# Optimization experiments

Hardware: AMD Instinct MI355X
Metric: run time of the kernel (lower is better)

The kernel has to match this reference:

```python
import jax, jax.numpy as jnp
import numpy as np

B, S, D_IN, D_OUT = 2, 4096, 512, 512


def setup_inputs() -> dict:
    key = jax.random.key(0)
    k1, k2, k3, k4 = jax.random.split(key, 4)
    x = jax.random.normal(k1, (B, S, D_IN), dtype=jnp.float32)
    # weights stored as [d_in, d_out] so projection is x @ W
    W_query = jax.random.normal(k2, (D_IN, D_OUT), dtype=jnp.float32) * (D_IN ** -0.5)
    W_key = jax.random.normal(k3, (D_IN, D_OUT), dtype=jnp.float32) * (D_IN ** -0.5)
    W_value = jax.random.normal(k4, (D_IN, D_OUT), dtype=jnp.float32) * (D_IN ** -0.5)
    return {"x": x, "W_query": W_query, "W_key": W_key, "W_value": W_value}


def reference(x, W_query, W_key, W_value):
    # Faithful to source: masked_fill is called non-in-place and its result
    # discarded, so NO causal mask is actually applied. Dropout prob = 0.0.
    d_out = W_query.shape[-1]
    q = jnp.einsum('bsi,io->bso', x, W_query)  # [B,S,D_OUT]
    k = jnp.einsum('bsi,io->bso', x, W_key)
    v = jnp.einsum('bsi,io->bso', x, W_value)
    scores = jnp.einsum('bqd,bkd->bqk', q, k) / jnp.sqrt(jnp.float32(d_out))
    weights = jax.nn.softmax(scores, axis=-1)  # [B,S,S]
    context = jnp.einsum('bqk,bkd->bqd', weights, v)  # [B,S,D_OUT]
    return context
```

## Files before the change

kernel.cpp:

```cpp
#include <hip/hip_runtime.h>
#include <cstdint>
#include <cstddef>

typedef unsigned short u16;
typedef __attribute__((ext_vector_type(8))) short bf16x8;
typedef __attribute__((ext_vector_type(4))) float f32x4;

struct alignas(8) u16x4_t { u16 x, y, z, w; };

__device__ __forceinline__ u16 f2bf(float f) {
  uint32_t u = __builtin_bit_cast(uint32_t, f);
  u += 0x7FFFu + ((u >> 16) & 1u);
  return (u16)(u >> 16);
}
__device__ __forceinline__ float bf2f(u16 h) {
  uint32_t u = ((uint32_t)h) << 16;
  return __builtin_bit_cast(float, u);
}

__device__ __forceinline__ void g2l16(const u16* g, u16* l) {
  __builtin_amdgcn_global_load_lds(
      (const __attribute__((address_space(1))) void*)g,
      (__attribute__((address_space(3))) void*)l, 16, 0, 0);
}

#define S_WAITCNT_VM(N) \
  __builtin_amdgcn_s_waitcnt((((N) & 0xF)) | (0x7 << 4) | (0xF << 8) | ((((N) >> 4) & 3) << 14))
#define S_WAITCNT_LGKM0 __builtin_amdgcn_s_waitcnt(0xC07F)

template <int DEPTH, int BM, int BN>
__device__ __forceinline__ void gemm_bt_pipe(
    const u16* __restrict__ A, const u16* __restrict__ Bt,
    int lda, int ldb, int kIters, int m0, int n0,
    u16* sh, f32x4 (&acc)[BM / 32][BN / 32]) {
  constexpr int MI = BM / 32;
  constexpr int NI = BN / 32;
  constexpr int T = (BM + BN) / 64;
  constexpr int SLOT = (BM + BN) * 32;
  const int tid = threadIdx.x;
  const int lane = tid & 63, wave = tid >> 6;
  const int wm = wave >> 1, wn = wave & 1, lr = lane & 15, quad = lane >> 4;

  const u16* gp[T];
#pragma unroll
  for (int t = 0; t < T; ++t) {
    const int c = t * 256 + wave * 64 + lane;
    if (c < BM * 4) {
      const int r = c >> 2;
      const int s = (c & 3) ^ ((r >> 1) & 3);
      gp[t] = A + (size_t)(m0 + r) * lda + s * 8;
    } else {
      const int cb = c - BM * 4;
      const int r = cb >> 2;
      const int s = (cb & 3) ^ ((r >> 1) & 3);
      gp[t] = Bt + (size_t)(n0 + r) * ldb + s * 8;
    }
  }
  const int wo = wave * 512;

  auto issue = [&](int slot, int kb) {
    u16* s = sh + slot * SLOT;
#pragma unroll
    for (int t = 0; t < T; ++t)
      g2l16(gp[t] + kb, s + t * 2048 + wo);
  };

#pragma unroll
  for (int p = 0; p < DEPTH; ++p)
    issue(p, (p < kIters ? p : kIters - 1) * 32);

  const int xq = (quad ^ ((lr >> 1) & 3)) * 8;
  const int arow = wm * (BM / 2) + lr;
  const int brow = wn * (BN / 2) + lr;

  bf16x8 af[MI], b0[NI], b1[NI];
  S_WAITCNT_VM(T * (DEPTH - 1));
  __builtin_amdgcn_s_barrier();
#pragma unroll
  for (int ni = 0; ni < NI; ++ni)
    b0[ni] = *(const bf16x8*)(sh + BM * 32 + ((brow + ni * 16) * 32 + xq));
#pragma unroll
  for (int mi = 0; mi < MI; ++mi)
    af[mi] = *(const bf16x8*)(sh + ((arow + mi * 16) * 32 + xq));

  auto step = [&](int kt, bf16x8 (&bc)[NI], bf16x8 (&bn)[NI]) {
    S_WAITCNT_VM(T * (DEPTH - 2));
    __builtin_amdgcn_s_barrier();
    const int nx = (kt + 1 < kIters) ? kt + 1 : kIters - 1;
    u16* s1 = sh + (nx % DEPTH) * SLOT;
#pragma unroll
    for (int ni = 0; ni < NI; ++ni)
      bn[ni] = *(const bf16x8*)(s1 + BM * 32 + ((brow + ni * 16) * 32 + xq));
    __builtin_amdgcn_s_setprio(1);
#pragma unroll
    for (int mi = 0; mi < MI; ++mi) {
#pragma unroll
      for (int ni = 0; ni < NI; ++ni)
        acc[mi][ni] = __builtin_amdgcn_mfma_f32_16x16x32_bf16(af[mi], bc[ni], acc[mi][ni], 0, 0, 0);
      af[mi] = *(const bf16x8*)(s1 + ((arow + mi * 16) * 32 + xq));
    }
    __builtin_amdgcn_s_setprio(0);
    __builtin_amdgcn_s_barrier();
    const int kn = kt + DEPTH;
    issue(kn % DEPTH, (kn < kIters ? kn : kIters - 1) * 32);
  };

  for (int kt = 0; kt + 2 <= kIters; kt += 2) {
    step(kt, b0, b1);
    step(kt + 1, b1, b0);
  }
}

template <int BM, int BN>
__device__ __forceinline__ void gemm_bt_8w_4ph(
    const u16* __restrict__ A, const u16* __restrict__ Bt,
    int lda, int ldb, int kIters, int m0, int n0,
    u16* sh, f32x4 (&acc)[BM / 32][BN / 64]) {
  constexpr int T = (BM + BN) / 128;
  constexpr int SLOT = (BM + BN) * 32;
  const int tid = threadIdx.x;
  const int lane = tid & 63, wave = tid >> 6;
  const int wm = wave >> 2, wn = wave & 3, lr = lane & 15, quad = lane >> 4;

  const u16* gp[T];
#pragma unroll
  for (int t = 0; t < T; ++t) {
    const int c = t * 512 + wave * 64 + lane;
    if (c < BM * 4) {
      const int r = c >> 2;
      const int s = (c & 3) ^ ((r >> 1) & 3);
      gp[t] = A + (size_t)(m0 + r) * lda + s * 8;
    } else {
      const int cb = c - BM * 4;
      const int r = cb >> 2;
      const int s = (cb & 3) ^ ((r >> 1) & 3);
      gp[t] = Bt + (size_t)(n0 + r) * ldb + s * 8;
    }
  }
  const int wo = wave * 512;

#pragma unroll
  for (int p = 0; p < 2; ++p)
#pragma unroll
    for (int t = 0; t < T; ++t)
      g2l16(gp[t] + p * 32, sh + p * SLOT + t * 4096 + wo);
  S_WAITCNT_VM(4);
  __builtin_amdgcn_s_barrier();

  const int xq = (quad ^ ((lr >> 1) & 3)) * 8;
  const int abase = (wm * (BM / 2) + lr) * 32 + xq;
  const int bbase = BM * 32 + (wn * (BN / 4) + lr) * 32 + xq;

  int si = 0, s2 = 2;
  for (int kt = 0; kt < kIters; ++kt) {
    u16* slot = sh + si * SLOT;
    const int kn = kt + 2;
    const int kb = (kn < kIters ? kn : kIters - 1) * 32;
    u16* st = sh + s2 * SLOT + wo;

    bf16x8 a0[4], b0[4];
#pragma unroll
    for (int i = 0; i < 4; ++i)
      a0[i] = *(const bf16x8*)(slot + abase + i * 512);
#pragma unroll
    for (int j = 0; j < 4; ++j)
      b0[j] = *(const bf16x8*)(slot + bbase + j * 512);
    g2l16(gp[0] + kb, st);
    g2l16(gp[1] + kb, st + 4096);
    __builtin_amdgcn_s_barrier();
    S_WAITCNT_LGKM0;
    __builtin_amdgcn_s_setprio(1);
#pragma unroll
    for (int i = 0; i < 4; ++i)
#pragma unroll
      for (int j = 0; j < 4; ++j)
        acc[i][j] = __builtin_amdgcn_mfma_f32_16x16x32_bf16(a0[i], b0[j], acc[i][j], 0, 0, 0);
    __builtin_amdgcn_s_setprio(0);
    __builtin_amdgcn_s_barrier();
#pragma unroll
    for (int i = 0; i < 4; ++i)
      a0[i] = *(const bf16x8*)(slot + abase + (4 + i) * 512);
    g2l16(gp[2] + kb, st + 8192);
    g2l16(gp[3] + kb, st + 12288);
    __builtin_amdgcn_s_barrier();
    S_WAITCNT_LGKM0;
    __builtin_amdgcn_s_setprio(1);
#pragma unroll
    for (int i = 0; i < 4; ++i)
#pragma unroll
      for (int j = 0; j < 4; ++j)
        acc[4 + i][j] = __builtin_amdgcn_mfma_f32_16x16x32_bf16(a0[i], b0[j], acc[4 + i][j], 0, 0, 0);
    __builtin_amdgcn_s_setprio(0);
    S_WAITCNT_VM(4);
    __builtin_amdgcn_s_barrier();
    si = si == 2 ? 0 : si + 1;
    s2 = s2 == 2 ? 0 : s2 + 1;
  }
}

#define ZERO_ACC4(acc)                        \
  _Pragma("unroll") for (int mi = 0; mi < 4; ++mi) \
  _Pragma("unroll") for (int ni = 0; ni < 4; ++ni) \
      acc[mi][ni] = f32x4{0.f, 0.f, 0.f, 0.f};

template <int MI>
__device__ __forceinline__ void epilogue_ct16(
    const f32x4 (&acc)[MI][4], u16* __restrict__ base, int m0w, int n0w,
    int ld, int lane, bool do_exp, float scale, float* rs) {
  const int lr = lane & 15, quad = lane >> 4;
  const int j = quad >> 1, par = quad & 1;
#pragma unroll
  for (int mp = 0; mp < MI / 2; ++mp) {
#pragma unroll
    for (int ni = 0; ni < 4; ++ni) {
      uint32_t p0[2], p1[2];
#pragma unroll
      for (int h = 0; h < 2; ++h) {
        const f32x4 v = acc[mp * 2 + h][ni];
        float e0, e1, e2, e3;
        if (do_exp) {
          e0 = __expf(v[0] * scale); e1 = __expf(v[1] * scale);
          e2 = __expf(v[2] * scale); e3 = __expf(v[3] * scale);
        } else {
          e0 = v[0]; e1 = v[1]; e2 = v[2]; e3 = v[3];
        }
        const u16 h0 = f2bf(e0), h1 = f2bf(e1), h2 = f2bf(e2), h3 = f2bf(e3);
        p0[h] = (uint32_t)h0 | ((uint32_t)h1 << 16);
        p1[h] = (uint32_t)h2 | ((uint32_t)h3 << 16);
        if (rs) rs[ni] += bf2f(h0) + bf2f(h1) + bf2f(h2) + bf2f(h3);
      }
      const uint32_t s0 = par ? p0[0] : p0[1];
      const uint32_t s1 = par ? p1[0] : p1[1];
      const uint32_t r0 = (uint32_t)__shfl_xor((int)s0, 16);
      const uint32_t r1 = (uint32_t)__shfl_xor((int)s1, 16);
      uint4 st;
      if (!par) { st.x = p0[0]; st.y = p1[0]; st.z = r0;    st.w = r1;    }
      else      { st.x = r0;    st.y = r1;    st.z = p0[1]; st.w = p1[1]; }
      const int m = m0w + 16 * (mp * 2 + par) + 8 * j;
      const int n = n0w + ni * 16 + lr;
      *(uint4*)(base + (size_t)n * ld + m) = st;
    }
  }
}

__global__ __launch_bounds__(256) void prep_kernel(
    const float* __restrict__ x, u16* __restrict__ Xb,
    const float* __restrict__ W0, const float* __restrict__ W1,
    const float* __restrict__ W2, u16* __restrict__ Wt,
    float* __restrict__ L) {
  __shared__ float tile[32][33];
  const int id = blockIdx.x;
  if (id < 4096) {
    const int i = (id * 256 + threadIdx.x) * 4;
    const float4 v = *(const float4*)(x + i);
    u16x4_t h;
    h.x = f2bf(v.x); h.y = f2bf(v.y); h.z = f2bf(v.z); h.w = f2bf(v.w);
    *(u16x4_t*)(Xb + i) = h;
    return;
  }
  if (id >= 4864) {
    L[(id - 4864) * 256 + threadIdx.x] = 0.f;
    return;
  }
  const int t = id - 4096;
  const int wz = t >> 8, rem = t & 255;
  const float* W = wz == 0 ? W0 : (wz == 1 ? W1 : W2);
  u16* out = Wt + (size_t)wz * 512 * 512;
  const int bx = (rem & 15) * 32;
  const int by = (rem >> 4) * 32;
  const int tx = threadIdx.x & 31, ty = threadIdx.x >> 5;
#pragma unroll
  for (int i = 0; i < 32; i += 8)
    tile[ty + i][tx] = W[(size_t)(by + ty + i) * 512 + bx + tx];
  __syncthreads();
#pragma unroll
  for (int i = 0; i < 32; i += 8)
    out[(size_t)(bx + ty + i) * 512 + by + tx] = f2bf(tile[tx][ty + i]);
}

__global__ __launch_bounds__(256) void qkv_kernel(
    const u16* __restrict__ Xb, const u16* __restrict__ Wt,
    u16* __restrict__ Qb, u16* __restrict__ Kb, u16* __restrict__ Vt) {
  __shared__ u16 sh[3 * 8192];
  const int z = blockIdx.z;
  int m0, n0;
  const u16 *A, *Bt;
  if (z < 2) {
    m0 = blockIdx.y * 128;
    n0 = blockIdx.x * 128;
    A = Wt + (size_t)z * 512 * 512;
    Bt = Xb;
  } else {
    m0 = blockIdx.x * 128;
    n0 = blockIdx.y * 128;
    A = Xb;
    Bt = Wt + (size_t)2 * 512 * 512;
  }
  f32x4 acc[4][4];
  ZERO_ACC4(acc);
  gemm_bt_pipe<3, 128, 128>(A, Bt, 512, 512, 16, m0, n0, sh, acc);

  const int lane = threadIdx.x & 63, wave = threadIdx.x >> 6;
  const int wm = wave >> 1, wn = wave & 1;
  if (z < 2) {
    epilogue_ct16<4>(acc, z == 0 ? Qb : Kb, m0 + wm * 64, n0 + wn * 64, 512,
                     lane, false, 1.f, nullptr);
  } else {
    const int bb = m0 >> 12;
    epilogue_ct16<4>(acc, Vt + (size_t)bb * 512 * 4096,
                     (m0 & 4095) + wm * 64, n0 + wn * 64, 4096,
                     lane, false, 1.f, nullptr);
  }
}

__global__ __launch_bounds__(512, 2) void scores_kernel(
    const u16* __restrict__ Qb, const u16* __restrict__ Kb,
    u16* __restrict__ P, float* __restrict__ L) {
  extern __shared__ u16 sh[];
  const int id = blockIdx.x;
  const int b = id >> 8;
  const int r = id & 255;
  const int j = r >> 3;
  const int qx = (r & 7) * 2 + (j >> 4);
  const int ky = j & 15;
  const int m0 = ky * 256;
  const int n0 = qx * 256;
  f32x4 acc[8][4];
#pragma unroll
  for (int mi = 0; mi < 8; ++mi)
#pragma unroll
    for (int ni = 0; ni < 4; ++ni)
      acc[mi][ni] = f32x4{0.f, 0.f, 0.f, 0.f};
  gemm_bt_8w_4ph<256, 256>(Kb + (size_t)b * 4096 * 512,
                           Qb + (size_t)b * 4096 * 512,
                           512, 512, 16, m0, n0, sh, acc);

  const int lane = threadIdx.x & 63, wave = threadIdx.x >> 6;
  const int wm = wave >> 2, wn = wave & 3, lr = lane & 15, quad = lane >> 4;
  const float scale = 0.04419417382415922f;
  u16* Pb = P + (size_t)b * 4096 * 4096;

  float rs[4] = {0.f, 0.f, 0.f, 0.f};
  epilogue_ct16<8>(acc, Pb, m0 + wm * 128, n0 + wn * 64, 4096, lane, true,
                   scale, rs);

#pragma unroll
  for (int ni = 0; ni < 4; ++ni) {
    float v = rs[ni];
    v += __shfl_xor(v, 16);
    v += __shfl_xor(v, 32);
    if (quad == 0)
      atomicAdd(&L[b * 4096 + n0 + wn * 64 + ni * 16 + lr], v);
  }
}

__global__ __launch_bounds__(256) void pv_kernel(
    const u16* __restrict__ P, const u16* __restrict__ Vt,
    float* __restrict__ part0, float* __restrict__ out) {
  __shared__ u16 sh[3 * 8192];
  const int b = blockIdx.z;
  const int id = blockIdx.x;
  const int ntile = (id >> 3) & 3;
  const int rest = (id & 7) | ((id >> 5) << 3);
  const int mtile = rest & 31;
  const int ks = rest >> 5;
  const int m0 = mtile * 128;
  const int n0 = ntile * 128;
  const int k0 = ks * 2048;
  f32x4 acc[4][4];
  ZERO_ACC4(acc);
  gemm_bt_pipe<3, 128, 128>(P + (size_t)b * 4096 * 4096 + k0,
                            Vt + (size_t)b * 512 * 4096 + k0,
                            4096, 4096, 64, m0, n0, sh, acc);

  const int lane = threadIdx.x & 63, wave = threadIdx.x >> 6;
  const int wm = wave >> 1, wn = wave & 1, lr = lane & 15, quad = lane >> 4;
  float* dst = ks ? out : part0;
#pragma unroll
  for (int mi = 0; mi < 4; ++mi) {
    const int row = m0 + wm * 64 + mi * 16 + quad * 4;
#pragma unroll
    for (int ni = 0; ni < 4; ++ni) {
      const int col = n0 + wn * 64 + ni * 16 + lr;
#pragma unroll
      for (int i = 0; i < 4; ++i)
        dst[(size_t)b * 2097152 + (size_t)(row + i) * 512 + col] = acc[mi][ni][i];
    }
  }
}

__global__ __launch_bounds__(256) void reduce_kernel(
    const float* __restrict__ part0, const float* __restrict__ L,
    float* __restrict__ out) {
  const int i = (blockIdx.x * 256 + threadIdx.x) * 4;
  const float rinv = 1.0f / L[i >> 9];
  const float4 a = *(const float4*)(out + i);
  const float4 p = *(const float4*)(part0 + i);
  float4 r;
  r.x = (a.x + p.x) * rinv; r.y = (a.y + p.y) * rinv;
  r.z = (a.z + p.z) * rinv; r.w = (a.w + p.w) * rinv;
  *(float4*)(out + i) = r;
}

extern "C" void kernel_launch(void* const* d_in, const int* in_sizes, int n_in,
                              void* d_out, int out_size, void* d_ws, size_t ws_size,
                              hipStream_t stream) {
  const float* x  = (const float*)d_in[0];
  const float* Wq = (const float*)d_in[1];
  const float* Wk = (const float*)d_in[2];
  const float* Wv = (const float*)d_in[3];
  float* out = (float*)d_out;
  char* ws = (char*)d_ws;
  u16* Xb = (u16*)(ws);
  u16* Qb = (u16*)(ws + 8388608);
  u16* Kb = (u16*)(ws + 16777216);
  u16* Vt = (u16*)(ws + 25165824);
  u16* Wt = (u16*)(ws + 33554432);
  u16* P  = (u16*)(ws + 35127296);
  float* L = (float*)(ws + 102236160);
  float* part0 = (float*)(ws + 8388608);

  static bool attr_set = false;
  if (!attr_set) {
    hipFuncSetAttribute(reinterpret_cast<const void*>(scores_kernel),
                        hipFuncAttributeMaxDynamicSharedMemorySize, 98304);
    attr_set = true;
  }

  prep_kernel<<<4896, 256, 0, stream>>>(x, Xb, Wq, Wk, Wv, Wt, L);
  qkv_kernel<<<dim3(64, 4, 3), 256, 0, stream>>>(Xb, Wt, Qb, Kb, Vt);
  scores_kernel<<<512, 512, 98304, stream>>>(Qb, Kb, P, L);
  pv_kernel<<<dim3(256, 1, 2), 256, 0, stream>>>(P, Vt, part0, out);
  reduce_kernel<<<4096, 256, 0, stream>>>(part0, L, out);
}
```

Measured before the change: 189.9 us.

## Drop split-K in PV, fuse normalization into epilogue, widen QKV tiles

Result: slower. 197.6 us (+4.1%).

```diff
diff --git a/kernel.cpp b/kernel.cpp
--- a/kernel.cpp
+++ b/kernel.cpp
@@ -72,6 +72,89 @@
   const int xq = (quad ^ ((lr >> 1) & 3)) * 8;
   const int arow = wm * (BM / 2) + lr;
   const int brow = wn * (BN / 2) + lr;
+
+  bf16x8 af[MI], b0[NI], b1[NI];
+  S_WAITCNT_VM(T * (DEPTH - 1));
+  __builtin_amdgcn_s_barrier();
+#pragma unroll
+  for (int ni = 0; ni < NI; ++ni)
+    b0[ni] = *(const bf16x8*)(sh + BM * 32 + ((brow + ni * 16) * 32 + xq));
+#pragma unroll
+  for (int mi = 0; mi < MI; ++mi)
+    af[mi] = *(const bf16x8*)(sh + ((arow + mi * 16) * 32 + xq));
+
+  auto step = [&](int kt, bf16x8 (&bc)[NI], bf16x8 (&bn)[NI]) {
+    S_WAITCNT_VM(T * (DEPTH - 2));
+    __builtin_amdgcn_s_barrier();
+    const int nx = (kt + 1 < kIters) ? kt + 1 : kIters - 1;
+    u16* s1 = sh + (nx % DEPTH) * SLOT;
+#pragma unroll
+    for (int ni = 0; ni < NI; ++ni)
+      bn[ni] = *(const bf16x8*)(s1 + BM * 32 + ((brow + ni * 16) * 32 + xq));
+    __builtin_amdgcn_s_setprio(1);
+#pragma unroll
+    for (int mi = 0; mi < MI; ++mi) {
+#pragma unroll
+      for (int ni = 0; ni < NI; ++ni)
+        acc[mi][ni] = __builtin_amdgcn_mfma_f32_16x16x32_bf16(af[mi], bc[ni], acc[mi][ni], 0, 0, 0);
+      af[mi] = *(const bf16x8*)(s1 + ((arow + mi * 16) * 32 + xq));
+    }
+    __builtin_amdgcn_s_setprio(0);
+    __builtin_amdgcn_s_barrier();
+    const int kn = kt + DEPTH;
+    issue(kn % DEPTH, (kn < kIters ? kn : kIters - 1) * 32);
+  };
+
+  for (int kt = 0; kt + 2 <= kIters; kt += 2) {
+    step(kt, b0, b1);
+    step(kt + 1, b1, b0);
+  }
+}
+
+template <int DEPTH, int BM, int BN>
+__device__ __forceinline__ void gemm_bt_pipe_w8(
+    const u16* __restrict__ A, const u16* __restrict__ Bt,
+    int lda, int ldb, int kIters, int m0, int n0,
+    u16* sh, f32x4 (&acc)[BM / 32][BN / 64]) {
+  constexpr int MI = BM / 32;
+  constexpr int NI = BN / 64;
+  constexpr int T = (BM + BN) / 128;
+  constexpr int SLOT = (BM + BN) * 32;
+  const int tid = threadIdx.x;
+  const int lane = tid & 63, wave = tid >> 6;
+  const int wm = wave >> 2, wn = wave & 3, lr = lane & 15, quad = lane >> 4;
+
+  const u16* gp[T];
+#pragma unroll
+  for (int t = 0; t < T; ++t) {
+    const int c = t * 512 + wave * 64 + lane;
+    if (c < BM * 4) {
+      const int r = c >> 2;
+      const int s = (c & 3) ^ ((r >> 1) & 3);
+      gp[t] = A + (size_t)(m0 + r) * lda + s * 8;
+    } else {
+      const int cb = c - BM * 4;
+      const int r = cb >> 2;
+      const int s = (cb & 3) ^ ((r >> 1) & 3);
+      gp[t] = Bt + (size_t)(n0 + r) * ldb + s * 8;
+    }
+  }
+  const int wo = wave * 512;
+
+  auto issue = [&](int slot, int kb) {
+    u16* s = sh + slot * SLOT;
+#pragma unroll
+    for (int t = 0; t < T; ++t)
+      g2l16(gp[t] + kb, s + t * 4096 + wo);
+  };
+
+#pragma unroll
+  for (int p = 0; p < DEPTH; ++p)
+    issue(p, (p < kIters ? p : kIters - 1) * 32);
+
+  const int xq = (quad ^ ((lr >> 1) & 3)) * 8;
+  const int arow = wm * (BM / 2) + lr;
+  const int brow = wn * (BN / 4) + lr;
 
   bf16x8 af[MI], b0[NI], b1[NI];
   S_WAITCNT_VM(T * (DEPTH - 1));
@@ -278,33 +361,36 @@
     out[(size_t)(bx + ty + i) * 512 + by + tx] = f2bf(tile[tx][ty + i]);
 }
 
-__global__ __launch_bounds__(256) void qkv_kernel(
+__global__ __launch_bounds__(512) void qkv_kernel(
     const u16* __restrict__ Xb, const u16* __restrict__ Wt,
     u16* __restrict__ Qb, u16* __restrict__ Kb, u16* __restrict__ Vt) {
-  __shared__ u16 sh[3 * 8192];
-  const int z = blockIdx.z;
+  extern __shared__ u16 sh[];
+  const int id = blockIdx.x;
   int m0, n0;
   const u16 *A, *Bt;
-  if (z < 2) {
-    m0 = blockIdx.y * 128;
-    n0 = blockIdx.x * 128;
-    A = Wt + (size_t)z * 512 * 512;
+  const bool isV = id >= 256;
+  if (!isV) {
+    const int q = id & 127;
+    m0 = (q >> 5) * 128;
+    n0 = (q & 31) * 256;
+    A = Wt + (size_t)(id >> 7) * 512 * 512;
     Bt = Xb;
   } else {
-    m0 = blockIdx.x * 128;
-    n0 = blockIdx.y * 128;
+    const int v = id - 256;
+    m0 = (v >> 1) * 128;
+    n0 = (v & 1) * 256;
     A = Xb;
     Bt = Wt + (size_t)2 * 512 * 512;
   }
   f32x4 acc[4][4];
   ZERO_ACC4(acc);
-  gemm_bt_pipe<3, 128, 128>(A, Bt, 512, 512, 16, m0, n0, sh, acc);
+  gemm_bt_pipe_w8<3, 128, 256>(A, Bt, 512, 512, 16, m0, n0, sh, acc);
 
   const int lane = threadIdx.x & 63, wave = threadIdx.x >> 6;
-  const int wm = wave >> 1, wn = wave & 1;
-  if (z < 2) {
-    epilogue_ct16<4>(acc, z == 0 ? Qb : Kb, m0 + wm * 64, n0 + wn * 64, 512,
-                     lane, false, 1.f, nullptr);
+  const int wm = wave >> 2, wn = wave & 3;
+  if (!isV) {
+    epilogue_ct16<4>(acc, (id >> 7) == 0 ? Qb : Kb, m0 + wm * 64, n0 + wn * 64,
+                     512, lane, false, 1.f, nullptr);
   } else {
     const int bb = m0 >> 12;
     epilogue_ct16<4>(acc, Vt + (size_t)bb * 512 * 4096,
@@ -356,50 +442,39 @@
 
 __global__ __launch_bounds__(256) void pv_kernel(
     const u16* __restrict__ P, const u16* __restrict__ Vt,
-    float* __restrict__ part0, float* __restrict__ out) {
+    const float* __restrict__ L, float* __restrict__ out) {
   __shared__ u16 sh[3 * 8192];
-  const int b = blockIdx.z;
   const int id = blockIdx.x;
-  const int ntile = (id >> 3) & 3;
-  const int rest = (id & 7) | ((id >> 5) << 3);
-  const int mtile = rest & 31;
-  const int ks = rest >> 5;
+  const int xcd = id & 7, s = id >> 3;
+  const int g = s >> 2, ntile = s & 3;
+  const int G = xcd + 8 * g;
+  const int b = G & 1;
+  const int mtile = G >> 1;
   const int m0 = mtile * 128;
   const int n0 = ntile * 128;
-  const int k0 = ks * 2048;
   f32x4 acc[4][4];
   ZERO_ACC4(acc);
-  gemm_bt_pipe<3, 128, 128>(P + (size_t)b * 4096 * 4096 + k0,
-                            Vt + (size_t)b * 512 * 4096 + k0,
-                            4096, 4096, 64, m0, n0, sh, acc);
+  gemm_bt_pipe<3, 128, 128>(P + (size_t)b * 4096 * 4096,
+                            Vt + (size_t)b * 512 * 4096,
+                            4096, 4096, 128, m0, n0, sh, acc);
 
   const int lane = threadIdx.x & 63, wave = threadIdx.x >> 6;
   const int wm = wave >> 1, wn = wave & 1, lr = lane & 15, quad = lane >> 4;
-  float* dst = ks ? out : part0;
+  const float* Lb = L + b * 4096;
 #pragma unroll
   for (int mi = 0; mi < 4; ++mi) {
     const int row = m0 + wm * 64 + mi * 16 + quad * 4;
 #pragma unroll
-    for (int ni = 0; ni < 4; ++ni) {
-      const int col = n0 + wn * 64 + ni * 16 + lr;
-#pragma unroll
-      for (int i = 0; i < 4; ++i)
-        dst[(size_t)b * 2097152 + (size_t)(row + i) * 512 + col] = acc[mi][ni][i];
-    }
-  }
-}
-
-__global__ __launch_bounds__(256) void reduce_kernel(
-    const float* __restrict__ part0, const float* __restrict__ L,
-    float* __restrict__ out) {
-  const int i = (blockIdx.x * 256 + threadIdx.x) * 4;
-  const float rinv = 1.0f / L[i >> 9];
-  const float4 a = *(const float4*)(out + i);
-  const float4 p = *(const float4*)(part0 + i);
-  float4 r;
-  r.x = (a.x + p.x) * rinv; r.y = (a.y + p.y) * rinv;
-  r.z = (a.z + p.z) * rinv; r.w = (a.w + p.w) * rinv;
-  *(float4*)(out + i) = r;
+    for (int i = 0; i < 4; ++i) {
+      const float rinv = 1.0f / Lb[row + i];
+#pragma unroll
+      for (int ni = 0; ni < 4; ++ni) {
+        const int col = n0 + wn * 64 + ni * 16 + lr;
+        out[(size_t)b * 2097152 + (size_t)(row + i) * 512 + col] =
+            acc[mi][ni][i] * rinv;
+      }
+    }
+  }
 }
 
 extern "C" void kernel_launch(void* const* d_in, const int* in_sizes, int n_in,
@@ -418,18 +493,18 @@
   u16* Wt = (u16*)(ws + 33554432);
   u16* P  = (u16*)(ws + 35127296);
   float* L = (float*)(ws + 102236160);
-  float* part0 = (float*)(ws + 8388608);
 
   static bool attr_set = false;
   if (!attr_set) {
     hipFuncSetAttribute(reinterpret_cast<const void*>(scores_kernel),
                         hipFuncAttributeMaxDynamicSharedMemorySize, 98304);
+    hipFuncSetAttribute(reinterpret_cast<const void*>(qkv_kernel),
+                        hipFuncAttributeMaxDynamicSharedMemorySize, 73728);
     attr_set = true;
   }
 
   prep_kernel<<<4896, 256, 0, stream>>>(x, Xb, Wq, Wk, Wv, Wt, L);
-  qkv_kernel<<<dim3(64, 4, 3), 256, 0, stream>>>(Xb, Wt, Qb, Kb, Vt);
+  qkv_kernel<<<384, 512, 73728, stream>>>(Xb, Wt, Qb, Kb, Vt);
   scores_kernel<<<512, 512, 98304, stream>>>(Qb, Kb, P, L);
-  pv_kernel<<<dim3(256, 1, 2), 256, 0, stream>>>(P, Vt, part0, out);
-  reduce_kernel<<<4096, 256, 0, stream>>>(part0, L, out);
-}
+  pv_kernel<<<256, 256, 0, stream>>>(P, Vt, L, out);
+}
```

## Fuse split-K reduction and normalization into PV kernel via in-block LDS reduce

Applied to the files above, without the earlier changes.

After: 182.4 us (median of 2 runs). -4.0%, faster.

```diff
diff --git a/kernel.cpp b/kernel.cpp
--- a/kernel.cpp
+++ b/kernel.cpp
@@ -32,12 +32,11 @@
 __device__ __forceinline__ void gemm_bt_pipe(
     const u16* __restrict__ A, const u16* __restrict__ Bt,
     int lda, int ldb, int kIters, int m0, int n0,
-    u16* sh, f32x4 (&acc)[BM / 32][BN / 32]) {
+    u16* sh, f32x4 (&acc)[BM / 32][BN / 32], int tid) {
   constexpr int MI = BM / 32;
   constexpr int NI = BN / 32;
   constexpr int T = (BM + BN) / 64;
   constexpr int SLOT = (BM + BN) * 32;
-  const int tid = threadIdx.x;
   const int lane = tid & 63, wave = tid >> 6;
   const int wm = wave >> 1, wn = wave & 1, lr = lane & 15, quad = lane >> 4;
 
@@ -298,7 +297,7 @@
   }
   f32x4 acc[4][4];
   ZERO_ACC4(acc);
-  gemm_bt_pipe<3, 128, 128>(A, Bt, 512, 512, 16, m0, n0, sh, acc);
+  gemm_bt_pipe<3, 128, 128>(A, Bt, 512, 512, 16, m0, n0, sh, acc, threadIdx.x);
 
   const int lane = threadIdx.x & 63, wave = threadIdx.x >> 6;
   const int wm = wave >> 1, wn = wave & 1;
@@ -354,52 +353,67 @@
   }
 }
 
-__global__ __launch_bounds__(256) void pv_kernel(
+__global__ __launch_bounds__(512) void pv_kernel(
     const u16* __restrict__ P, const u16* __restrict__ Vt,
-    float* __restrict__ part0, float* __restrict__ out) {
-  __shared__ u16 sh[3 * 8192];
-  const int b = blockIdx.z;
+    const float* __restrict__ L, float* __restrict__ out) {
+  extern __shared__ u16 sh[];
   const int id = blockIdx.x;
-  const int ntile = (id >> 3) & 3;
-  const int rest = (id & 7) | ((id >> 5) << 3);
-  const int mtile = rest & 31;
-  const int ks = rest >> 5;
+  const int xcd = id & 7, s = id >> 3;
+  const int g = s >> 2, ntile = s & 3;
+  const int G = xcd + 8 * g;
+  const int b = G & 1;
+  const int mtile = G >> 1;
   const int m0 = mtile * 128;
   const int n0 = ntile * 128;
-  const int k0 = ks * 2048;
+
+  const int wave8 = threadIdx.x >> 6;
+  const int kg = wave8 >> 2;
+  const int tid4 = threadIdx.x & 255;
+  const int k0 = kg * 2048;
+
   f32x4 acc[4][4];
   ZERO_ACC4(acc);
   gemm_bt_pipe<3, 128, 128>(P + (size_t)b * 4096 * 4096 + k0,
                             Vt + (size_t)b * 512 * 4096 + k0,
-                            4096, 4096, 64, m0, n0, sh, acc);
-
-  const int lane = threadIdx.x & 63, wave = threadIdx.x >> 6;
-  const int wm = wave >> 1, wn = wave & 1, lr = lane & 15, quad = lane >> 4;
-  float* dst = ks ? out : part0;
-#pragma unroll
-  for (int mi = 0; mi < 4; ++mi) {
-    const int row = m0 + wm * 64 + mi * 16 + quad * 4;
-#pragma unroll
-    for (int ni = 0; ni < 4; ++ni) {
-      const int col = n0 + wn * 64 + ni * 16 + lr;
-#pragma unroll
-      for (int i = 0; i < 4; ++i)
-        dst[(size_t)b * 2097152 + (size_t)(row + i) * 512 + col] = acc[mi][ni][i];
+                            4096, 4096, 64, m0, n0,
+                            sh + kg * 24576, acc, tid4);
+
+  S_WAITCNT_VM(0);
+  __builtin_amdgcn_s_barrier();
+
+  const int iw = wave8 & 3;
+  const int lane = threadIdx.x & 63;
+  float* cs = (float*)sh;
+  float* reg = cs + iw * 4160 + lane * 65;
+
+  if (kg == 1) {
+#pragma unroll
+    for (int mi = 0; mi < 4; ++mi)
+#pragma unroll
+      for (int ni = 0; ni < 4; ++ni)
+#pragma unroll
+        for (int i = 0; i < 4; ++i)
+          reg[mi * 16 + ni * 4 + i] = acc[mi][ni][i];
+  }
+  __syncthreads();
+  if (kg == 0) {
+    const int wm = iw >> 1, wn = iw & 1, lr = lane & 15, quad = lane >> 4;
+    const float* Lb = L + b * 4096;
+#pragma unroll
+    for (int mi = 0; mi < 4; ++mi) {
+      const int row = m0 + wm * 64 + mi * 16 + quad * 4;
+#pragma unroll
+      for (int i = 0; i < 4; ++i) {
+        const float rinv = 1.0f / Lb[row + i];
+#pragma unroll
+        for (int ni = 0; ni < 4; ++ni) {
+          const int col = n0 + wn * 64 + ni * 16 + lr;
+          out[(size_t)b * 2097152 + (size_t)(row + i) * 512 + col] =
+              (acc[mi][ni][i] + reg[mi * 16 + ni * 4 + i]) * rinv;
+        }
+      }
     }
   }
-}
-
-__global__ __launch_bounds__(256) void reduce_kernel(
-    const float* __restrict__ part0, const float* __restrict__ L,
-    float* __restrict__ out) {
-  const int i = (blockIdx.x * 256 + threadIdx.x) * 4;
-  const float rinv = 1.0f / L[i >> 9];
-  const float4 a = *(const float4*)(out + i);
-  const float4 p = *(const float4*)(part0 + i);
-  float4 r;
-  r.x = (a.x + p.x) * rinv; r.y = (a.y + p.y) * rinv;
-  r.z = (a.z + p.z) * rinv; r.w = (a.w + p.w) * rinv;
-  *(float4*)(out + i) = r;
 }
 
 extern "C" void kernel_launch(void* const* d_in, const int* in_sizes, int n_in,
@@ -418,18 +432,18 @@
   u16* Wt = (u16*)(ws + 33554432);
   u16* P  = (u16*)(ws + 35127296);
   float* L = (float*)(ws + 102236160);
-  float* part0 = (float*)(ws + 8388608);
 
   static bool attr_set = false;
   if (!attr_set) {
     hipFuncSetAttribute(reinterpret_cast<const void*>(scores_kernel),
                         hipFuncAttributeMaxDynamicSharedMemorySize, 98304);
+    hipFuncSetAttribute(reinterpret_cast<const void*>(pv_kernel),
+                        hipFuncAttributeMaxDynamicSharedMemorySize, 98304);
     attr_set = true;
   }
 
   prep_kernel<<<4896, 256, 0, stream>>>(x, Xb, Wq, Wk, Wv, Wt, L);
   qkv_kernel<<<dim3(64, 4, 3), 256, 0, stream>>>(Xb, Wt, Qb, Kb, Vt);
   scores_kernel<<<512, 512, 98304, stream>>>(Qb, Kb, P, L);
-  pv_kernel<<<dim3(256, 1, 2), 256, 0, stream>>>(P, Vt, part0, out);
-  reduce_kernel<<<4096, 256, 0, stream>>>(part0, L, out);
-}
+  pv_kernel<<<256, 512, 98304, stream>>>(P, Vt, L, out);
+}
```
